# Kernel optimization log

Hardware: AMD Instinct MI355X
Metric: run time of the kernel (lower is better)

Reference implementation:

```python
import jax, jax.numpy as jnp
import numpy as np

B, S, IN, E, H, FF, L = 8, 1024, 128, 512, 8, 2048, 4
HD = E // H
EPS = 1e-5


def make_pe(seq_len, d_model):
    position = np.arange(seq_len, dtype=np.float32)[:, None]
    div_term = np.exp(np.arange(0, d_model, 2, dtype=np.float32) * (-np.log(10000.0) / d_model))
    pe = np.zeros((seq_len, d_model), dtype=np.float32)
    pe[:, 0::2] = np.sin(position * div_term)
    pe[:, 1::2] = np.cos(position * div_term)
    return jnp.asarray(pe)


def setup_inputs() -> dict:
    key = jax.random.key(0)
    ks = jax.random.split(key, 16)
    s = 0.02
    return {
        "src": jax.random.normal(ks[0], (B, S, IN), jnp.float32),
        "distances": jax.random.uniform(ks[1], (B, S, S), jnp.float32),
        "proj_w": jax.random.normal(ks[2], (E, IN), jnp.float32) * s,
        "proj_b": jnp.zeros((E,), jnp.float32),
        "bn_g": jnp.ones((E,), jnp.float32),
        "bn_b": jnp.zeros((E,), jnp.float32),
        "in_proj_w": jax.random.normal(ks[3], (3 * E, E), jnp.float32) * s,
        "in_proj_b": jnp.zeros((3 * E,), jnp.float32),
        "dist_scale": jnp.array(1.0, jnp.float32),
        "lin1_w": jax.random.normal(ks[4], (FF, E), jnp.float32) * s,
        "lin1_b": jnp.zeros((FF,), jnp.float32),
        "lin2_w": jax.random.normal(ks[5], (E, FF), jnp.float32) * s,
        "lin2_b": jnp.zeros((E,), jnp.float32),
        "n1_g": jnp.ones((E,), jnp.float32),
        "n1_b": jnp.zeros((E,), jnp.float32),
        "n2_g": jnp.ones((E,), jnp.float32),
        "n2_b": jnp.zeros((E,), jnp.float32),
    }


def layernorm(x, g, b):
    m = jnp.mean(x, axis=-1, keepdims=True)
    v = jnp.var(x, axis=-1, keepdims=True)
    return (x - m) * jax.lax.rsqrt(v + EPS) * g + b


def reference(src, distances, proj_w, proj_b, bn_g, bn_b, in_proj_w, in_proj_b,
              dist_scale, lin1_w, lin1_b, lin2_w, lin2_b, n1_g, n1_b, n2_g, n2_b):
    # input projection
    x = jnp.einsum('bsi,ei->bse', src, proj_w) + proj_b  # [B,S,E]
    # BatchNorm1d over flattened (B*S) dim, training-mode batch stats
    xf = x.reshape(-1, E)
    mu = jnp.mean(xf, axis=0)
    var = jnp.var(xf, axis=0)
    x = ((xf - mu) * jax.lax.rsqrt(var + EPS) * bn_g + bn_b).reshape(B, S, E)
    # positional encoding
    x = x + make_pe(S, E)[None]
    # distance bias (same for every layer)
    dmax = jnp.max(distances, axis=-1, keepdims=True)
    dist_bias = jnp.exp(dist_scale * (1.0 - distances / dmax))  # [B,S,S]
    scale = 1.0 / jnp.sqrt(jnp.float32(HD))
    # num_layers iterations of the SAME (shared-parameter) layer
    for _ in range(L):
        qkv = jnp.einsum('bse,fe->bsf', x, in_proj_w) + in_proj_b  # [B,S,3E]
        q, k, v = jnp.split(qkv, 3, axis=-1)
        q = q.reshape(B, S, H, HD).transpose(0, 2, 1, 3)
        k = k.reshape(B, S, H, HD).transpose(0, 2, 1, 3)
        scores = jnp.einsum('bhqd,bhkd->bhqk', q, k) * scale  # [B,H,S,S]
        attn = jax.nn.softmax(scores, axis=-1)
        avg_w = jnp.mean(attn, axis=1)  # head-averaged weights [B,S,S]
        w = avg_w * dist_bias
        w = w / jnp.sum(w, axis=-1, keepdims=True)
        # NOTE: original bmm uses raw layer input as value (no V/out projection)
        attn_out = jnp.einsum('bqk,bke->bqe', w, x)
        x = layernorm(x + attn_out, n1_g, n1_b)
        ff = jnp.einsum('bsf,ef->bse', jax.nn.relu(jnp.einsum('bse,fe->bsf', x, lin1_w) + lin1_b), lin2_w) + lin2_b
        x = layernorm(x + ff, n2_g, n2_b)
    return x
```

## Files before the change

kernel.cpp:

```cpp
#include <hip/hip_runtime.h>
#include <hip/hip_bf16.h>
#include <math.h>

#define Bz 8
#define Sz 1024
#define INz 128
#define Ez 512
#define Hz 8
#define HDz 64
#define FFz 2048
#define Lz 4
#define Nz (Bz*Sz)
#define EPSf 1e-5f

typedef __attribute__((ext_vector_type(8))) short short8;
typedef __attribute__((ext_vector_type(4))) float floatx4;
#define MFMA16(a,b,c) __builtin_amdgcn_mfma_f32_16x16x32_bf16(a,b,c,0,0,0)

typedef __hip_bfloat16 bf16;

__device__ inline float b2f(bf16 v) { return __bfloat162float(v); }
__device__ inline bf16 f2b(float v) { return __float2bfloat16(v); }

__global__ __launch_bounds__(256) void cast_f2b(const float* __restrict__ in,
    bf16* __restrict__ out, int n)
{
  int i = blockIdx.x * 256 + threadIdx.x;
  if (i < n) out[i] = f2b(in[i]);
}

__global__ __launch_bounds__(256) void gemm_bt(
    const bf16* __restrict__ A, const bf16* __restrict__ Wm,
    const float* __restrict__ bias, float* __restrict__ Cf,
    bf16* __restrict__ Cb, const float* __restrict__ rowscale,
    int M, int N, int K, long sA, long sW, long sC, int relu)
{
  int z = blockIdx.z;
  A  += (size_t)z * sA;
  Wm += (size_t)z * sW;
  if (rowscale) rowscale += (size_t)z * M;
  size_t cbase = (size_t)z * sC;
  int bm = blockIdx.y * 128, bn = blockIdx.x * 128;
  __shared__ bf16 As[128][72];
  __shared__ bf16 Bs[128][72];
  int t = threadIdx.x, wave = t >> 6, lane = t & 63;
  int wm = (wave >> 1) * 64, wn = (wave & 1) * 64;
  int fr = lane & 15, fo = (lane >> 4) * 8;
  floatx4 acc[4][4];
  #pragma unroll
  for (int i = 0; i < 4; ++i)
    #pragma unroll
    for (int j = 0; j < 4; ++j) acc[i][j] = (floatx4){0.f, 0.f, 0.f, 0.f};

  for (int k0 = 0; k0 < K; k0 += 64) {
    #pragma unroll
    for (int i = 0; i < 4; ++i) {
      int idx = i * 256 + t, row = idx >> 3, c4 = idx & 7;
      *(float4*)&As[row][c4 * 8] = *(const float4*)(A  + (size_t)(bm + row) * K + k0 + c4 * 8);
      *(float4*)&Bs[row][c4 * 8] = *(const float4*)(Wm + (size_t)(bn + row) * K + k0 + c4 * 8);
    }
    __syncthreads();
    #pragma unroll
    for (int ks = 0; ks < 2; ++ks) {
      short8 af[4], bfv[4];
      #pragma unroll
      for (int rt = 0; rt < 4; ++rt) af[rt]  = *(const short8*)&As[wm + rt * 16 + fr][ks * 32 + fo];
      #pragma unroll
      for (int ct = 0; ct < 4; ++ct) bfv[ct] = *(const short8*)&Bs[wn + ct * 16 + fr][ks * 32 + fo];
      #pragma unroll
      for (int rt = 0; rt < 4; ++rt)
        #pragma unroll
        for (int ct = 0; ct < 4; ++ct)
          acc[rt][ct] = MFMA16(af[rt], bfv[ct], acc[rt][ct]);
    }
    __syncthreads();
  }
  #pragma unroll
  for (int rt = 0; rt < 4; ++rt) {
    #pragma unroll
    for (int r = 0; r < 4; ++r) {
      int row = bm + wm + rt * 16 + (lane >> 4) * 4 + r;
      float rs = rowscale ? (1.f / rowscale[row]) : 1.f;
      #pragma unroll
      for (int ct = 0; ct < 4; ++ct) {
        int col = bn + wn + ct * 16 + fr;
        float v = acc[rt][ct][r] + (bias ? bias[col] : 0.f);
        if (relu) v = fmaxf(v, 0.f);
        v *= rs;
        if (Cf) Cf[cbase + (size_t)row * N + col] = v;
        if (Cb) Cb[cbase + (size_t)row * N + col] = f2b(v);
      }
    }
  }
}

__global__ __launch_bounds__(256) void bn_stats(const float* __restrict__ x, float* __restrict__ st)
{
  int c = blockIdx.x;
  float s = 0.f, q = 0.f;
  for (int r = threadIdx.x; r < Nz; r += 256) {
    float v = x[(size_t)r * Ez + c];
    s += v; q += v * v;
  }
  for (int o = 32; o; o >>= 1) { s += __shfl_down(s, o); q += __shfl_down(q, o); }
  __shared__ float shs[4], shq[4];
  int w = threadIdx.x >> 6;
  if ((threadIdx.x & 63) == 0) { shs[w] = s; shq[w] = q; }
  __syncthreads();
  if (threadIdx.x == 0) {
    s = shs[0] + shs[1] + shs[2] + shs[3];
    q = shq[0] + shq[1] + shq[2] + shq[3];
    float mu = s / (float)Nz;
    float var = q / (float)Nz - mu * mu;
    st[c] = mu;
    st[Ez + c] = rsqrtf(var + EPSf);
  }
}

__global__ __launch_bounds__(256) void bn_apply_pe(const float* __restrict__ x0,
    const float* __restrict__ st, const float* __restrict__ g,
    const float* __restrict__ b, float* __restrict__ x, bf16* __restrict__ xb)
{
  int idx = blockIdx.x * 256 + threadIdx.x;
  int c = idx & (Ez - 1);
  int r = idx >> 9;
  int s = r & (Sz - 1);
  float dt = expf((float)(c & ~1) * (-9.210340371976184f / (float)Ez));
  float ang = (float)s * dt;
  float pe = (c & 1) ? cosf(ang) : sinf(ang);
  float mu = st[c], rs = st[Ez + c];
  float v = (x0[idx] - mu) * rs * g[c] + b[c] + pe;
  x[idx] = v;
  xb[idx] = f2b(v);
}

__global__ __launch_bounds__(256) void dist_bias_k(const float* __restrict__ dist,
    const float* __restrict__ dsc, bf16* __restrict__ db)
{
  size_t base = (size_t)blockIdx.x * Sz;
  float m = -1e30f;
  for (int j = threadIdx.x; j < Sz; j += 256) m = fmaxf(m, dist[base + j]);
  for (int o = 32; o; o >>= 1) m = fmaxf(m, __shfl_down(m, o));
  __shared__ float sh[4];
  if ((threadIdx.x & 63) == 0) sh[threadIdx.x >> 6] = m;
  __syncthreads();
  m = fmaxf(fmaxf(sh[0], sh[1]), fmaxf(sh[2], sh[3]));
  float sc = dsc[0];
  float inv = 1.f / m;
  for (int j = threadIdx.x; j < Sz; j += 256)
    db[base + j] = f2b(expf(sc * (1.f - dist[base + j] * inv)));
}

__global__ __launch_bounds__(256) void transpose_xb(const bf16* __restrict__ xb,
    bf16* __restrict__ xT)
{
  int b = blockIdx.z, e0 = blockIdx.y * 32, s0 = blockIdx.x * 32;
  __shared__ bf16 T[32][40];
  int t = threadIdx.x, row = t >> 3, c = t & 7;
  *(ushort4*)&T[row][c * 4] = *(const ushort4*)(xb + (size_t)(b * Sz + s0 + row) * Ez + e0 + c * 4);
  __syncthreads();
  ushort4 v;
  unsigned short* vp = (unsigned short*)&v;
  #pragma unroll
  for (int i = 0; i < 4; ++i) vp[i] = *(const unsigned short*)&T[c * 4 + i][row];
  *(ushort4*)(xT + ((size_t)b * Ez + e0 + row) * Sz + s0 + c * 4) = v;
}

__global__ __launch_bounds__(256) void attn_stats2(const bf16* __restrict__ qk,
    float* __restrict__ stats)
{
  int qt = blockIdx.x, h = blockIdx.y, b = blockIdx.z;
  int q0 = qt * 64;
  __shared__ bf16 Qs[64][72];
  __shared__ bf16 Ks[128][72];
  int t = threadIdx.x, wave = t >> 6, lane = t & 63;
  int fr = lane & 15, fo = (lane >> 4) * 8;
  #pragma unroll
  for (int i = 0; i < 2; ++i) {
    int idx = i * 256 + t, row = idx >> 3, c4 = idx & 7;
    *(float4*)&Qs[row][c4 * 8] =
      *(const float4*)(qk + (size_t)(b * Sz + q0 + row) * 1024 + h * 64 + c4 * 8);
  }
  __syncthreads();
  short8 aq0 = *(const short8*)&Qs[wave * 16 + fr][fo];
  short8 aq1 = *(const short8*)&Qs[wave * 16 + fr][32 + fo];
  float m_run[4] = {-1e30f, -1e30f, -1e30f, -1e30f};
  float z_run[4] = {0.f, 0.f, 0.f, 0.f};
  for (int k0 = 0; k0 < Sz; k0 += 128) {
    __syncthreads();
    #pragma unroll
    for (int i = 0; i < 4; ++i) {
      int idx = i * 256 + t, row = idx >> 3, c4 = idx & 7;
      *(float4*)&Ks[row][c4 * 8] =
        *(const float4*)(qk + (size_t)(b * Sz + k0 + row) * 1024 + 512 + h * 64 + c4 * 8);
    }
    __syncthreads();
    float sc[8][4];
    #pragma unroll
    for (int j = 0; j < 8; ++j) {
      floatx4 a4 = (floatx4){0.f, 0.f, 0.f, 0.f};
      short8 b0 = *(const short8*)&Ks[j * 16 + fr][fo];
      short8 b1 = *(const short8*)&Ks[j * 16 + fr][32 + fo];
      a4 = MFMA16(aq0, b0, a4);
      a4 = MFMA16(aq1, b1, a4);
      #pragma unroll
      for (int r = 0; r < 4; ++r) sc[j][r] = a4[r] * 0.125f;
    }
    #pragma unroll
    for (int r = 0; r < 4; ++r) {
      float vm = sc[0][r];
      #pragma unroll
      for (int j = 1; j < 8; ++j) vm = fmaxf(vm, sc[j][r]);
      #pragma unroll
      for (int o = 1; o < 16; o <<= 1) vm = fmaxf(vm, __shfl_xor(vm, o, 16));
      float mn = fmaxf(m_run[r], vm);
      float zb = 0.f;
      #pragma unroll
      for (int j = 0; j < 8; ++j) zb += __expf(sc[j][r] - mn);
      #pragma unroll
      for (int o = 1; o < 16; o <<= 1) zb += __shfl_xor(zb, o, 16);
      z_run[r] = z_run[r] * __expf(m_run[r] - mn) + zb;
      m_run[r] = mn;
    }
  }
  if (fr == 0) {
    int qb = q0 + wave * 16 + (lane >> 4) * 4;
    #pragma unroll
    for (int r = 0; r < 4; ++r) {
      size_t o = ((size_t)(b * Hz + h) * Sz + qb + r) * 2;
      stats[o] = m_run[r];
      stats[o + 1] = z_run[r];
    }
  }
}

__global__ __launch_bounds__(256) void scores_bias(const bf16* __restrict__ qk,
    const bf16* __restrict__ db, const float* __restrict__ stats,
    bf16* __restrict__ aw)
{
  int kt = blockIdx.x, qt = blockIdx.y, b = blockIdx.z;
  int q0 = qt * 32, k0 = kt * 32;
  __shared__ bf16 Qs[32][520];
  __shared__ bf16 Ks[32][520];
  __shared__ float mS[32][8], ziS[32][8];
  int t = threadIdx.x, wave = t >> 6, lane = t & 63;
  int fr = lane & 15, fo = (lane >> 4) * 8;
  #pragma unroll
  for (int i = 0; i < 8; ++i) {
    int idx = i * 256 + t, row = idx >> 6, c4 = idx & 63;
    *(float4*)&Qs[row][c4 * 8] = *(const float4*)(qk + (size_t)(b * Sz + q0 + row) * 1024 + c4 * 8);
    *(float4*)&Ks[row][c4 * 8] = *(const float4*)(qk + (size_t)(b * Sz + k0 + row) * 1024 + 512 + c4 * 8);
  }
  {
    int q = t >> 3, h = t & 7;
    size_t o = ((size_t)(b * Hz + h) * Sz + q0 + q) * 2;
    mS[q][h] = stats[o];
    ziS[q][h] = 1.f / stats[o + 1];
  }
  __syncthreads();
  int wq = (wave >> 1) * 16, wk = (wave & 1) * 16;
  floatx4 acch[8];
  #pragma unroll
  for (int h = 0; h < 8; ++h) {
    acch[h] = (floatx4){0.f, 0.f, 0.f, 0.f};
    #pragma unroll
    for (int ks = 0; ks < 2; ++ks) {
      short8 a = *(const short8*)&Qs[wq + fr][h * 64 + ks * 32 + fo];
      short8 bb = *(const short8*)&Ks[wk + fr][h * 64 + ks * 32 + fo];
      acch[h] = MFMA16(a, bb, acch[h]);
    }
  }
  #pragma unroll
  for (int r = 0; r < 4; ++r) {
    int qloc = wq + (lane >> 4) * 4 + r;
    int kloc = wk + fr;
    float p = 0.f;
    #pragma unroll
    for (int h = 0; h < 8; ++h)
      p += __expf(acch[h][r] * 0.125f - mS[qloc][h]) * ziS[qloc][h];
    size_t off = (size_t)(b * Sz + q0 + qloc) * Sz + k0 + kloc;
    p *= 0.125f * b2f(db[off]);
    aw[off] = f2b(p);
  }
}

__global__ __launch_bounds__(256) void rowsum(const bf16* __restrict__ aw,
    float* __restrict__ den)
{
  size_t base = (size_t)blockIdx.x * Sz;
  int t = threadIdx.x;
  ushort4 u = *(const ushort4*)(aw + base + t * 4);
  float s = __uint_as_float((unsigned)u.x << 16) + __uint_as_float((unsigned)u.y << 16)
          + __uint_as_float((unsigned)u.z << 16) + __uint_as_float((unsigned)u.w << 16);
  for (int o = 32; o; o >>= 1) s += __shfl_down(s, o);
  __shared__ float sh[4];
  if ((t & 63) == 0) sh[t >> 6] = s;
  __syncthreads();
  if (t == 0) den[blockIdx.x] = sh[0] + sh[1] + sh[2] + sh[3];
}

__global__ __launch_bounds__(256) void add_ln(const float* __restrict__ xin,
    const float* __restrict__ dly, const float* __restrict__ g,
    const float* __restrict__ bb, float* __restrict__ xout, bf16* __restrict__ xbout)
{
  size_t base = (size_t)blockIdx.x * Ez;
  int t = threadIdx.x;
  float a0 = xin[base + t] + dly[base + t];
  float a1 = xin[base + t + 256] + dly[base + t + 256];
  float s = a0 + a1, q = a0 * a0 + a1 * a1;
  for (int o = 32; o; o >>= 1) { s += __shfl_down(s, o); q += __shfl_down(q, o); }
  __shared__ float shs[4], shq[4];
  if ((t & 63) == 0) { shs[t >> 6] = s; shq[t >> 6] = q; }
  __syncthreads();
  s = shs[0] + shs[1] + shs[2] + shs[3];
  q = shq[0] + shq[1] + shq[2] + shq[3];
  float mu = s * (1.f / Ez);
  float var = q * (1.f / Ez) - mu * mu;
  float rs = rsqrtf(var + EPSf);
  float v0 = (a0 - mu) * rs * g[t] + bb[t];
  float v1 = (a1 - mu) * rs * g[t + 256] + bb[t + 256];
  xout[base + t] = v0;
  xout[base + t + 256] = v1;
  xbout[base + t] = f2b(v0);
  xbout[base + t + 256] = f2b(v1);
}

extern "C" void kernel_launch(void* const* d_in, const int* in_sizes, int n_in,
                              void* d_out, int out_size, void* d_ws, size_t ws_size,
                              hipStream_t stream)
{
  const float* src        = (const float*)d_in[0];
  const float* distances  = (const float*)d_in[1];
  const float* proj_w     = (const float*)d_in[2];
  const float* proj_b     = (const float*)d_in[3];
  const float* bn_g       = (const float*)d_in[4];
  const float* bn_b       = (const float*)d_in[5];
  const float* in_proj_w  = (const float*)d_in[6];
  const float* in_proj_b  = (const float*)d_in[7];
  const float* dist_scale = (const float*)d_in[8];
  const float* lin1_w     = (const float*)d_in[9];
  const float* lin1_b     = (const float*)d_in[10];
  const float* lin2_w     = (const float*)d_in[11];
  const float* lin2_b     = (const float*)d_in[12];
  const float* n1_g       = (const float*)d_in[13];
  const float* n1_b       = (const float*)d_in[14];
  const float* n2_g       = (const float*)d_in[15];
  const float* n2_b       = (const float*)d_in[16];

  float* x = (float*)d_out;

  float* stats = (float*)d_ws;
  float* den   = stats + 131072;
  float* bnst  = den + 8192;
  float* aout  = bnst + 1024;
  float* x0    = aout;
  bf16* db_b = (bf16*)(aout + (size_t)Nz * Ez);
  bf16* Rqk  = db_b + (size_t)Bz * Sz * Sz;
  bf16* qk   = Rqk;
  bf16* aw   = Rqk + (size_t)Nz * 1024;
  bf16* ff1  = Rqk;
  bf16* xb   = Rqk + (size_t)Nz * FFz;
  bf16* xT   = xb + (size_t)Nz * Ez;
  bf16* srcb = xT + (size_t)Bz * Ez * Sz;
  bf16* wpr  = srcb + (size_t)Nz * INz;
  bf16* wqk  = wpr + Ez * INz;
  bf16* wl1  = wqk + 1024 * Ez;
  bf16* wl2  = wl1 + FFz * Ez;

  cast_f2b<<<(Nz * INz) / 256, 256, 0, stream>>>(src, srcb, Nz * INz);
  cast_f2b<<<(Ez * INz + 255) / 256, 256, 0, stream>>>(proj_w, wpr, Ez * INz);
  cast_f2b<<<(1024 * Ez) / 256, 256, 0, stream>>>(in_proj_w, wqk, 1024 * Ez);
  cast_f2b<<<(FFz * Ez) / 256, 256, 0, stream>>>(lin1_w, wl1, FFz * Ez);
  cast_f2b<<<(Ez * FFz) / 256, 256, 0, stream>>>(lin2_w, wl2, Ez * FFz);

  gemm_bt<<<dim3(Ez / 128, Nz / 128, 1), 256, 0, stream>>>(
      srcb, wpr, proj_b, x0, nullptr, nullptr, Nz, Ez, INz, 0, 0, 0, 0);
  bn_stats<<<Ez, 256, 0, stream>>>(x0, bnst);
  bn_apply_pe<<<(Nz * Ez) / 256, 256, 0, stream>>>(x0, bnst, bn_g, bn_b, x, xb);
  dist_bias_k<<<Bz * Sz, 256, 0, stream>>>(distances, dist_scale, db_b);

  for (int l = 0; l < Lz; ++l) {
    transpose_xb<<<dim3(Sz / 32, Ez / 32, Bz), 256, 0, stream>>>(xb, xT);
    gemm_bt<<<dim3(1024 / 128, Nz / 128, 1), 256, 0, stream>>>(
        xb, wqk, in_proj_b, nullptr, qk, nullptr, Nz, 1024, Ez, 0, 0, 0, 0);
    attn_stats2<<<dim3(Sz / 64, Hz, Bz), 256, 0, stream>>>(qk, stats);
    scores_bias<<<dim3(Sz / 32, Sz / 32, Bz), 256, 0, stream>>>(qk, db_b, stats, aw);
    rowsum<<<Bz * Sz, 256, 0, stream>>>(aw, den);
    gemm_bt<<<dim3(Ez / 128, Sz / 128, Bz), 256, 0, stream>>>(
        aw, xT, nullptr, aout, nullptr, den,
        Sz, Ez, Sz, (long)Sz * Sz, (long)Ez * Sz, (long)Sz * Ez, 0);
    add_ln<<<Nz, 256, 0, stream>>>(x, aout, n1_g, n1_b, x, xb);
    gemm_bt<<<dim3(FFz / 128, Nz / 128, 1), 256, 0, stream>>>(
        xb, wl1, lin1_b, nullptr, ff1, nullptr, Nz, FFz, Ez, 0, 0, 0, 1);
    gemm_bt<<<dim3(Ez / 128, Nz / 128, 1), 256, 0, stream>>>(
        ff1, wl2, lin2_b, aout, nullptr, nullptr, Nz, Ez, FFz, 0, 0, 0, 0);
    add_ln<<<Nz, 256, 0, stream>>>(x, aout, n2_g, n2_b, x, xb);
  }
}
```

Before: 1.283 ms.

## Fuse biased attention weights, row sums and PV product into one kernel

Replaces the scores_bias, rowsum and batched gemm path with a single attn_pv kernel. Per 32-query tile it recomputes head-averaged probabilities, applies the distance bias, accumulates the row denominators and multiplies by x^T using MFMA. This avoids writing and re-reading the B*S*S bf16 weight matrix and drops two launches. The GEMM is also simplified and switched to direct global-to-LDS loads without padding, which may add LDS bank conflicts. The fused kernel launches only 256 blocks and uses serial k-loops with three barriers per step, so occupancy and latency hiding are a risk.

```diff
diff --git a/kernel.cpp b/kernel.cpp
--- a/kernel.cpp
+++ b/kernel.cpp
@@ -22,6 +22,12 @@
 __device__ inline float b2f(bf16 v) { return __bfloat162float(v); }
 __device__ inline bf16 f2b(float v) { return __float2bfloat16(v); }
 
+__device__ inline void gll16(const bf16* g, bf16* l) {
+  __builtin_amdgcn_global_load_lds(
+      (const __attribute__((address_space(1))) unsigned int*)g,
+      (__attribute__((address_space(3))) unsigned int*)l, 16, 0, 0);
+}
+
 __global__ __launch_bounds__(256) void cast_f2b(const float* __restrict__ in,
     bf16* __restrict__ out, int n)
 {
@@ -32,20 +38,15 @@
 __global__ __launch_bounds__(256) void gemm_bt(
     const bf16* __restrict__ A, const bf16* __restrict__ Wm,
     const float* __restrict__ bias, float* __restrict__ Cf,
-    bf16* __restrict__ Cb, const float* __restrict__ rowscale,
-    int M, int N, int K, long sA, long sW, long sC, int relu)
-{
-  int z = blockIdx.z;
-  A  += (size_t)z * sA;
-  Wm += (size_t)z * sW;
-  if (rowscale) rowscale += (size_t)z * M;
-  size_t cbase = (size_t)z * sC;
+    bf16* __restrict__ Cb, int M, int N, int K, int relu)
+{
   int bm = blockIdx.y * 128, bn = blockIdx.x * 128;
-  __shared__ bf16 As[128][72];
-  __shared__ bf16 Bs[128][72];
+  __shared__ bf16 As[128][64];
+  __shared__ bf16 Bs[128][64];
   int t = threadIdx.x, wave = t >> 6, lane = t & 63;
   int wm = (wave >> 1) * 64, wn = (wave & 1) * 64;
   int fr = lane & 15, fo = (lane >> 4) * 8;
+  int lrow = lane >> 3, lcol = (lane & 7) * 8;
   floatx4 acc[4][4];
   #pragma unroll
   for (int i = 0; i < 4; ++i)
@@ -54,10 +55,11 @@
 
   for (int k0 = 0; k0 < K; k0 += 64) {
     #pragma unroll
-    for (int i = 0; i < 4; ++i) {
-      int idx = i * 256 + t, row = idx >> 3, c4 = idx & 7;
-      *(float4*)&As[row][c4 * 8] = *(const float4*)(A  + (size_t)(bm + row) * K + k0 + c4 * 8);
-      *(float4*)&Bs[row][c4 * 8] = *(const float4*)(Wm + (size_t)(bn + row) * K + k0 + c4 * 8);
+    for (int c = 0; c < 4; ++c) {
+      int chunk = wave * 4 + c;
+      int row = chunk * 8 + lrow;
+      gll16(A  + (size_t)(bm + row) * K + k0 + lcol, &As[0][0] + chunk * 512);
+      gll16(Wm + (size_t)(bn + row) * K + k0 + lcol, &Bs[0][0] + chunk * 512);
     }
     __syncthreads();
     #pragma unroll
@@ -80,15 +82,13 @@
     #pragma unroll
     for (int r = 0; r < 4; ++r) {
       int row = bm + wm + rt * 16 + (lane >> 4) * 4 + r;
-      float rs = rowscale ? (1.f / rowscale[row]) : 1.f;
       #pragma unroll
       for (int ct = 0; ct < 4; ++ct) {
         int col = bn + wn + ct * 16 + fr;
         float v = acc[rt][ct][r] + (bias ? bias[col] : 0.f);
         if (relu) v = fmaxf(v, 0.f);
-        v *= rs;
-        if (Cf) Cf[cbase + (size_t)row * N + col] = v;
-        if (Cb) Cb[cbase + (size_t)row * N + col] = f2b(v);
+        if (Cf) Cf[(size_t)row * N + col] = v;
+        if (Cb) Cb[(size_t)row * N + col] = f2b(v);
       }
     }
   }
@@ -234,22 +234,29 @@
   }
 }
 
-__global__ __launch_bounds__(256) void scores_bias(const bf16* __restrict__ qk,
-    const bf16* __restrict__ db, const float* __restrict__ stats,
-    bf16* __restrict__ aw)
-{
-  int kt = blockIdx.x, qt = blockIdx.y, b = blockIdx.z;
-  int q0 = qt * 32, k0 = kt * 32;
-  __shared__ bf16 Qs[32][520];
+__global__ __launch_bounds__(256) void attn_pv(const bf16* __restrict__ qk,
+    const bf16* __restrict__ xT, const bf16* __restrict__ db,
+    const float* __restrict__ stats, float* __restrict__ aout)
+{
+  int qt = blockIdx.x, b = blockIdx.y;
+  int q0 = qt * 32;
+  __shared__ __align__(16) char smemQV[512 * 40 * 2];
+  bf16 (*Qs)[520] = (bf16(*)[520])smemQV;
+  bf16 (*Vs)[40]  = (bf16(*)[40])smemQV;
   __shared__ bf16 Ks[32][520];
+  __shared__ bf16 Ps[32][40];
   __shared__ float mS[32][8], ziS[32][8];
+  __shared__ float denS[32];
   int t = threadIdx.x, wave = t >> 6, lane = t & 63;
-  int fr = lane & 15, fo = (lane >> 4) * 8;
+  int fr = lane & 15, fq = lane >> 4;
+  int fo = fq * 8;
+  int wq = (wave >> 1) * 16, wk = (wave & 1) * 16;
+  int qg = wave >> 1, eg = wave & 1;
+
   #pragma unroll
   for (int i = 0; i < 8; ++i) {
     int idx = i * 256 + t, row = idx >> 6, c4 = idx & 63;
     *(float4*)&Qs[row][c4 * 8] = *(const float4*)(qk + (size_t)(b * Sz + q0 + row) * 1024 + c4 * 8);
-    *(float4*)&Ks[row][c4 * 8] = *(const float4*)(qk + (size_t)(b * Sz + k0 + row) * 1024 + 512 + c4 * 8);
   }
   {
     int q = t >> 3, h = t & 7;
@@ -257,46 +264,85 @@
     mS[q][h] = stats[o];
     ziS[q][h] = 1.f / stats[o + 1];
   }
-  __syncthreads();
-  int wq = (wave >> 1) * 16, wk = (wave & 1) * 16;
-  floatx4 acch[8];
+  if (t < 32) denS[t] = 0.f;
+  __syncthreads();
+
+  short8 qa[8][2];
   #pragma unroll
   for (int h = 0; h < 8; ++h) {
-    acch[h] = (floatx4){0.f, 0.f, 0.f, 0.f};
-    #pragma unroll
-    for (int ks = 0; ks < 2; ++ks) {
-      short8 a = *(const short8*)&Qs[wq + fr][h * 64 + ks * 32 + fo];
-      short8 bb = *(const short8*)&Ks[wk + fr][h * 64 + ks * 32 + fo];
-      acch[h] = MFMA16(a, bb, acch[h]);
-    }
-  }
-  #pragma unroll
-  for (int r = 0; r < 4; ++r) {
-    int qloc = wq + (lane >> 4) * 4 + r;
-    int kloc = wk + fr;
-    float p = 0.f;
-    #pragma unroll
-    for (int h = 0; h < 8; ++h)
-      p += __expf(acch[h][r] * 0.125f - mS[qloc][h]) * ziS[qloc][h];
-    size_t off = (size_t)(b * Sz + q0 + qloc) * Sz + k0 + kloc;
-    p *= 0.125f * b2f(db[off]);
-    aw[off] = f2b(p);
-  }
-}
-
-__global__ __launch_bounds__(256) void rowsum(const bf16* __restrict__ aw,
-    float* __restrict__ den)
-{
-  size_t base = (size_t)blockIdx.x * Sz;
-  int t = threadIdx.x;
-  ushort4 u = *(const ushort4*)(aw + base + t * 4);
-  float s = __uint_as_float((unsigned)u.x << 16) + __uint_as_float((unsigned)u.y << 16)
-          + __uint_as_float((unsigned)u.z << 16) + __uint_as_float((unsigned)u.w << 16);
-  for (int o = 32; o; o >>= 1) s += __shfl_down(s, o);
-  __shared__ float sh[4];
-  if ((t & 63) == 0) sh[t >> 6] = s;
-  __syncthreads();
-  if (t == 0) den[blockIdx.x] = sh[0] + sh[1] + sh[2] + sh[3];
+    qa[h][0] = *(const short8*)&Qs[wq + fr][h * 64 + fo];
+    qa[h][1] = *(const short8*)&Qs[wq + fr][h * 64 + 32 + fo];
+  }
+  __syncthreads();
+
+  floatx4 acc[16];
+  #pragma unroll
+  for (int j = 0; j < 16; ++j) acc[j] = (floatx4){0.f, 0.f, 0.f, 0.f};
+  float dacc[4] = {0.f, 0.f, 0.f, 0.f};
+
+  for (int k0 = 0; k0 < Sz; k0 += 32) {
+    #pragma unroll
+    for (int i = 0; i < 8; ++i) {
+      int idx = i * 256 + t, row = idx >> 6, c4 = idx & 63;
+      *(float4*)&Ks[row][c4 * 8] =
+        *(const float4*)(qk + (size_t)(b * Sz + k0 + row) * 1024 + 512 + c4 * 8);
+    }
+    #pragma unroll
+    for (int i = 0; i < 8; ++i) {
+      int idx = i * 256 + t, row = idx >> 2, c = idx & 3;
+      *(float4*)&Vs[row][c * 8] =
+        *(const float4*)(xT + ((size_t)b * Ez + row) * Sz + k0 + c * 8);
+    }
+    __syncthreads();
+    floatx4 acch[8];
+    #pragma unroll
+    for (int h = 0; h < 8; ++h) {
+      acch[h] = (floatx4){0.f, 0.f, 0.f, 0.f};
+      short8 kb0 = *(const short8*)&Ks[wk + fr][h * 64 + fo];
+      short8 kb1 = *(const short8*)&Ks[wk + fr][h * 64 + 32 + fo];
+      acch[h] = MFMA16(qa[h][0], kb0, acch[h]);
+      acch[h] = MFMA16(qa[h][1], kb1, acch[h]);
+    }
+    #pragma unroll
+    for (int r = 0; r < 4; ++r) {
+      int ql = wq + fq * 4 + r;
+      float p = 0.f;
+      #pragma unroll
+      for (int h = 0; h < 8; ++h)
+        p += __expf(acch[h][r] * 0.125f - mS[ql][h]) * ziS[ql][h];
+      p *= 0.125f;
+      p *= b2f(db[(size_t)(b * Sz + q0 + ql) * Sz + k0 + wk + fr]);
+      bf16 pb = f2b(p);
+      Ps[ql][wk + fr] = pb;
+      float v = b2f(pb);
+      #pragma unroll
+      for (int o = 1; o < 16; o <<= 1) v += __shfl_xor(v, o, 16);
+      dacc[r] += v;
+    }
+    __syncthreads();
+    short8 ap = *(const short8*)&Ps[qg * 16 + fr][fo];
+    #pragma unroll
+    for (int j = 0; j < 16; ++j) {
+      short8 bv = *(const short8*)&Vs[eg * 256 + j * 16 + fr][fo];
+      acc[j] = MFMA16(ap, bv, acc[j]);
+    }
+    __syncthreads();
+  }
+
+  if (fr == 0) {
+    #pragma unroll
+    for (int r = 0; r < 4; ++r) atomicAdd(&denS[wq + fq * 4 + r], dacc[r]);
+  }
+  __syncthreads();
+  #pragma unroll
+  for (int j = 0; j < 16; ++j) {
+    #pragma unroll
+    for (int r = 0; r < 4; ++r) {
+      int ql = qg * 16 + fq * 4 + r;
+      int col = eg * 256 + j * 16 + fr;
+      aout[(size_t)(b * Sz + q0 + ql) * Ez + col] = acc[j][r] / denS[ql];
+    }
+  }
 }
 
 __global__ __launch_bounds__(256) void add_ln(const float* __restrict__ xin,
@@ -357,7 +403,6 @@
   bf16* db_b = (bf16*)(aout + (size_t)Nz * Ez);
   bf16* Rqk  = db_b + (size_t)Bz * Sz * Sz;
   bf16* qk   = Rqk;
-  bf16* aw   = Rqk + (size_t)Nz * 1024;
   bf16* ff1  = Rqk;
   bf16* xb   = Rqk + (size_t)Nz * FFz;
   bf16* xT   = xb + (size_t)Nz * Ez;
@@ -373,27 +418,23 @@
   cast_f2b<<<(FFz * Ez) / 256, 256, 0, stream>>>(lin1_w, wl1, FFz * Ez);
   cast_f2b<<<(Ez * FFz) / 256, 256, 0, stream>>>(lin2_w, wl2, Ez * FFz);
 
-  gemm_bt<<<dim3(Ez / 128, Nz / 128, 1), 256, 0, stream>>>(
-      srcb, wpr, proj_b, x0, nullptr, nullptr, Nz, Ez, INz, 0, 0, 0, 0);
+  gemm_bt<<<dim3(Ez / 128, Nz / 128), 256, 0, stream>>>(
+      srcb, wpr, proj_b, x0, nullptr, Nz, Ez, INz, 0);
   bn_stats<<<Ez, 256, 0, stream>>>(x0, bnst);
   bn_apply_pe<<<(Nz * Ez) / 256, 256, 0, stream>>>(x0, bnst, bn_g, bn_b, x, xb);
   dist_bias_k<<<Bz * Sz, 256, 0, stream>>>(distances, dist_scale, db_b);
 
   for (int l = 0; l < Lz; ++l) {
     transpose_xb<<<dim3(Sz / 32, Ez / 32, Bz), 256, 0, stream>>>(xb, xT);
-    gemm_bt<<<dim3(1024 / 128, Nz / 128, 1), 256, 0, stream>>>(
-        xb, wqk, in_proj_b, nullptr, qk, nullptr, Nz, 1024, Ez, 0, 0, 0, 0);
+    gemm_bt<<<dim3(1024 / 128, Nz / 128), 256, 0, stream>>>(
+        xb, wqk, in_proj_b, nullptr, qk, Nz, 1024, Ez, 0);
     attn_stats2<<<dim3(Sz / 64, Hz, Bz), 256, 0, stream>>>(qk, stats);
-    scores_bias<<<dim3(Sz / 32, Sz / 32, Bz), 256, 0, stream>>>(qk, db_b, stats, aw);
-    rowsum<<<Bz * Sz, 256, 0, stream>>>(aw, den);
-    gemm_bt<<<dim3(Ez / 128, Sz / 128, Bz), 256, 0, stream>>>(
-        aw, xT, nullptr, aout, nullptr, den,
-        Sz, Ez, Sz, (long)Sz * Sz, (long)Ez * Sz, (long)Sz * Ez, 0);
+    attn_pv<<<dim3(Sz / 32, Bz), 256, 0, stream>>>(qk, xT, db_b, stats, aout);
     add_ln<<<Nz, 256, 0, stream>>>(x, aout, n1_g, n1_b, x, xb);
-    gemm_bt<<<dim3(FFz / 128, Nz / 128, 1), 256, 0, stream>>>(
-        xb, wl1, lin1_b, nullptr, ff1, nullptr, Nz, FFz, Ez, 0, 0, 0, 1);
-    gemm_bt<<<dim3(Ez / 128, Nz / 128, 1), 256, 0, stream>>>(
-        ff1, wl2, lin2_b, aout, nullptr, nullptr, Nz, Ez, FFz, 0, 0, 0, 0);
+    gemm_bt<<<dim3(FFz / 128, Nz / 128), 256, 0, stream>>>(
+        xb, wl1, lin1_b, nullptr, ff1, Nz, FFz, Ez, 1);
+    gemm_bt<<<dim3(Ez / 128, Nz / 128), 256, 0, stream>>>(
+        ff1, wl2, lin2_b, aout, nullptr, Nz, Ez, FFz, 0);
     add_ln<<<Nz, 256, 0, stream>>>(x, aout, n2_g, n2_b, x, xb);
   }
 }
```

Measured after the change: 1.706 ms. 33.0% more time.
